# Kernel optimization log

Measured on AMD Instinct MI355X. Metric: run time of the kernel, lower is better.

## Reference

```python
import jax, jax.numpy as jnp
import numpy as np

N, CIN, COUT, K, CSTYLE, H, W = 8, 512, 512, 3, 512, 64, 64
EPS = 1e-8
SQRT2 = 2.0 ** 0.5


def setup_inputs() -> dict:
    key = jax.random.key(0)
    ks = jax.random.split(key, 5)
    return {
        "x": jax.random.normal(ks[0], (N, CIN, H, W), jnp.float32),
        "style": jax.random.normal(ks[1], (N, CSTYLE), jnp.float32),
        "noise": jax.random.normal(ks[2], (N, 1, H, W), jnp.float32),
        "conv_weight": jax.random.normal(ks[3], (1, COUT, CIN, K, K), jnp.float32),
        "mod_weight": jax.random.normal(ks[4], (CIN, CSTYLE), jnp.float32) / np.float32(np.sqrt(CSTYLE)),
        "mod_bias": jnp.ones((CIN,), jnp.float32),
        "noise_weight": jnp.zeros((1,), jnp.float32),
        "act_bias": jnp.zeros((COUT,), jnp.float32),
    }


def reference(x, style, noise, conv_weight, mod_weight, mod_bias, noise_weight, act_bias):
    n = x.shape[0]
    # style modulation: linear(style) -> per-sample per-in-channel scale (style_bias=0)
    s = style @ mod_weight.T + mod_bias                       # (n, cin)
    # modulate shared weight (1, cout, cin, k, k) -> (n, cout, cin, k, k)
    w = conv_weight * s[:, None, :, None, None]
    # demodulate
    demod = jax.lax.rsqrt(jnp.sum(w * w, axis=(2, 3, 4)) + EPS)  # (n, cout)
    w = w * demod[:, :, None, None, None]
    # grouped conv: groups = batch
    w = w.reshape(n * COUT, CIN, K, K)
    xg = x.reshape(1, n * CIN, H, W)
    out = jax.lax.conv_general_dilated(
        xg, w,
        window_strides=(1, 1),
        padding=[(K // 2, K // 2), (K // 2, K // 2)],
        dimension_numbers=("NCHW", "OIHW", "NCHW"),
        feature_group_count=n,
    )
    out = out.reshape(n, COUT, H, W) * SQRT2
    # noise injection (scalar weight, broadcast noise)
    out = out + noise_weight[0] * noise
    # fused bias + leaky relu (slope 0.2)
    out = jax.nn.leaky_relu(out + act_bias[None, :, None, None], negative_slope=0.2)
    return out
```

## Files before the change

kernel.cpp:

```cpp
#include <hip/hip_runtime.h>
#include <hip/hip_bf16.h>
#include <stdint.h>


typedef __attribute__((ext_vector_type(8))) short short8;
typedef __attribute__((ext_vector_type(4))) float f32x4;
typedef __attribute__((ext_vector_type(16))) float f32x16;
typedef __attribute__((ext_vector_type(4))) unsigned int uint4v;
typedef __attribute__((ext_vector_type(2))) unsigned int uint2v;

__device__ __forceinline__ unsigned short f2bf(float f) {
  unsigned u = __builtin_bit_cast(unsigned, f);
  u += 0x7FFFu + ((u >> 16) & 1u);
  return (unsigned short)(u >> 16);
}

__device__ __forceinline__ void g2l16(const void* g, void* l) {
  __builtin_amdgcn_global_load_lds(
      (const __attribute__((address_space(1))) void*)g,
      (__attribute__((address_space(3))) void*)l, 16, 0, 0);
}

__global__ void k_pre(const float* __restrict__ style, const float* __restrict__ mw,
                      const float* __restrict__ mb, const float* __restrict__ cw,
                      float* __restrict__ s_out, float* __restrict__ wsq) {
  int t = threadIdx.x;
  int b = blockIdx.x;
  if (b < 1024) {
    int wid = b * 4 + (t >> 6);
    int lane = t & 63;
    int n = wid >> 9, ci = wid & 511;
    float sum = 0.f;
#pragma unroll
    for (int i = 0; i < 8; ++i) {
      int k = lane + i * 64;
      sum += style[n * 512 + k] * mw[ci * 512 + k];
    }
#pragma unroll
    for (int off = 32; off; off >>= 1) sum += __shfl_xor(sum, off, 64);
    if (lane == 0) s_out[wid] = sum + mb[ci];
  } else {
    int id = (b - 1024) * 256 + t;
    const float* p = cw + (size_t)id * 9;
    float a = 0.f;
#pragma unroll
    for (int j = 0; j < 9; ++j) a += p[j] * p[j];
    wsq[id] = a;
  }
}

__global__ void k_mid(const float* __restrict__ s, const float* __restrict__ wsq,
                      const float* __restrict__ x, const float* __restrict__ cw,
                      float* __restrict__ demod, unsigned short* __restrict__ Xp,
                      unsigned short* __restrict__ Wt) {
  __shared__ char smem[74240];
  int t = threadIdx.x;
  int b = blockIdx.x;
  if (b < 512) {
    int n = b >> 6, h = b & 63;
    short* ldsx = (short*)smem;
    float* sxf = (float*)(smem + 69632);
    sxf[t] = s[n * 512 + t];
    sxf[t + 256] = s[n * 512 + 256 + t];
    __syncthreads();
    const float* xb = x + ((size_t)n * 512) * 4096 + h * 64;
#pragma unroll
    for (int i = 0; i < 32; ++i) {
      int L = t + i * 256;
      int ci = L >> 4, q = L & 15;
      f32x4 v = *(const f32x4*)(xb + (size_t)ci * 4096 + q * 4);
      float sv = sxf[ci];
      uint2v o;
      o.x = f2bf(v.x * sv) | ((unsigned)f2bf(v.y * sv) << 16);
      o.y = f2bf(v.z * sv) | ((unsigned)f2bf(v.w * sv) << 16);
      *(uint2v*)(ldsx + ci * 68 + q * 4) = o;
    }
    __syncthreads();
    unsigned short* nb = Xp + (size_t)n * 2230272 + (size_t)(h + 1) * 33792;
#pragma unroll
    for (int r = 0; r < 16; ++r) {
      int u = t + r * 256;
      int cig = u >> 6, col = u & 63;
      unsigned v[8];
#pragma unroll
      for (int j = 0; j < 8; ++j)
        v[j] = (unsigned short)ldsx[(cig * 8 + j) * 68 + col];
      uint4v o;
      o.x = v[0] | (v[1] << 16);
      o.y = v[2] | (v[3] << 16);
      o.z = v[4] | (v[5] << 16);
      o.w = v[6] | (v[7] << 16);
      *(uint4v*)(nb + ((size_t)cig * 66 + col + 1) * 8) = o;
    }
  } else if (b < 1536) {
    int wid = (b - 512) * 4 + (t >> 6);
    int lane = t & 63;
    int n = wid >> 9, co = wid & 511;
    float sum = 0.f;
#pragma unroll
    for (int i = 0; i < 8; ++i) {
      int ci = lane + i * 64;
      float sv = s[n * 512 + ci];
      sum += sv * sv * wsq[co * 512 + ci];
    }
#pragma unroll
    for (int off = 32; off; off >>= 1) sum += __shfl_xor(sum, off, 64);
    if (lane == 0) demod[wid] = rsqrtf(sum + 1e-8f) * 1.41421356237309515f;
  } else if (b < 1792) {
    int bb = b - 1536;
    int cb = bb >> 4, kb = bb & 15;
    float* ldsf = (float*)smem;
#pragma unroll
    for (int i = 0; i < 36; ++i) {
      int idx = t + i * 256;
      int seg = idx / 288, off = idx - seg * 288;
      ldsf[seg * 289 + off] = cw[(size_t)(cb * 32 + seg) * 4608 + kb * 288 + off];
    }
    __syncthreads();
    unsigned short* ob = Wt + (size_t)(cb * 16 + kb) * 9216;
#pragma unroll
    for (int i = 0; i < 5; ++i) {
      int c = t + i * 256;
      if (c < 1152) {
        int co_rel = c & 31, lhi = (c >> 5) & 3, tap = c >> 7;
        unsigned v[8];
#pragma unroll
        for (int j = 0; j < 8; ++j)
          v[j] = f2bf(ldsf[co_rel * 289 + (lhi * 8 + j) * 9 + tap]);
        uint4v o;
        o.x = v[0] | (v[1] << 16);
        o.y = v[2] | (v[3] << 16);
        o.z = v[4] | (v[5] << 16);
        o.w = v[6] | (v[7] << 16);
        *(uint4v*)(ob + (size_t)c * 8) = o;
      }
    }
  } else {
    int bb = b - 1792;
    int n = bb / 17, part = bb % 17;
    uint4v z = (uint4v){0u, 0u, 0u, 0u};
    unsigned short* base = Xp + (size_t)n * 2230272;
#pragma unroll
    for (int i = 0; i < 4; ++i) {
      int id = part * 1024 + i * 256 + t;
      if (id < 16640) {
        size_t off;
        if (id < 8448) {
          int row = (id < 4224) ? 0 : 65;
          int c = id - ((id < 4224) ? 0 : 4224);
          off = (size_t)row * 33792 + (size_t)c * 8;
        } else {
          int id2 = id - 8448;
          int row = 1 + (id2 >> 7);
          int rem = id2 & 127;
          int klhi = rem >> 1;
          int col = (rem & 1) ? 65 : 0;
          off = (size_t)row * 33792 + ((size_t)klhi * 66 + col) * 8;
        }
        *(uint4v*)(base + off) = z;
      }
    }
  }
}

__global__ void __launch_bounds__(256, 3) k_conv(
    const unsigned short* __restrict__ Wt, const unsigned short* __restrict__ Xp,
    const float* __restrict__ demod, const float* __restrict__ noise,
    const float* __restrict__ nw_p, const float* __restrict__ act_bias,
    float* __restrict__ out) {
  __shared__ short lds_a[9216];
  __shared__ short lds_x[16896];
  int t = threadIdx.x;
  int wg = blockIdx.x;
  int n = wg & 7;
  int rem = wg >> 3;
  int cb = rem / 11;
  int bx = rem - cb * 11;
  int r0 = (bx < 10) ? bx * 6 : 58;
  int lane = t & 63, wv = t >> 6;
  int l31 = lane & 31, hi = lane >> 5;
  int ch = wv >> 1, rg = wv & 1;

  const unsigned short* abase = Wt + (size_t)cb * 16 * 9216;
  const unsigned short* xbase = Xp + (size_t)n * 2230272;
  int xoffg[9];
#pragma unroll
  for (int j = 0; j < 9; ++j) {
    int c = j * 256 + t;
    int r = c / 264, rc = c - r * 264;
    int off = (r0 + r) * 33792 + rc * 8;
    if (c >= 2112) off = 0;
    xoffg[j] = off;
  }

  f32x16 acc[3];
#pragma unroll
  for (int r = 0; r < 3; ++r)
#pragma unroll
    for (int q = 0; q < 16; ++q) acc[r][q] = 0.f;

  const int aoff = hi * 256 + l31 * 8;
  const int xb0 = hi * 528 + ch * 256 + l31 * 8;

  for (int kb = 0; kb < 16; ++kb) {
    __syncthreads();
    const char* ab = (const char*)(abase + (size_t)kb * 9216);
#pragma unroll
    for (int i = 0; i < 5; ++i) {
      int c = i * 256 + t;
      if (c < 1152) g2l16(ab + c * 16, (char*)lds_a + c * 16);
    }
#pragma unroll
    for (int j = 0; j < 9; ++j) {
      int c = j * 256 + t;
      if (c < 2112) g2l16(xbase + xoffg[j] + kb * 2112, (char*)lds_x + c * 16);
    }
    __syncthreads();

#pragma unroll
    for (int dw = 0; dw < 3; ++dw) {
      short8 bf[5][2];
#pragma unroll
      for (int rr = 0; rr < 5; ++rr)
#pragma unroll
        for (int ks = 0; ks < 2; ++ks)
          bf[rr][ks] = *(const short8*)(lds_x + (rg * 3 + rr) * 2112 + ks * 1056 +
                                        dw * 8 + xb0);
#pragma unroll
      for (int dh = 0; dh < 3; ++dh) {
        int tap = dh * 3 + dw;
#pragma unroll
        for (int ks = 0; ks < 2; ++ks) {
          short8 af = *(const short8*)(lds_a + tap * 1024 + ks * 512 + aoff);
#pragma unroll
          for (int r = 0; r < 3; ++r)
            acc[r] = __builtin_amdgcn_mfma_f32_32x32x16_bf16(af, bf[r + dh][ks],
                                                             acc[r], 0, 0, 0);
        }
      }
    }
  }

  float nw = nw_p[0];
  int col = ch * 32 + l31;
  f32x4 dm4[4], ab4[4];
#pragma unroll
  for (int q = 0; q < 4; ++q) {
    dm4[q] = *(const f32x4*)(demod + n * 512 + cb * 32 + q * 8 + hi * 4);
    ab4[q] = *(const f32x4*)(act_bias + cb * 32 + q * 8 + hi * 4);
  }
#pragma unroll
  for (int r = 0; r < 3; ++r) {
    int R = r0 + rg * 3 + r;
    float nz = nw * noise[((size_t)n * 64 + R) * 64 + col];
#pragma unroll
    for (int q = 0; q < 4; ++q) {
#pragma unroll
      for (int c = 0; c < 4; ++c) {
        int co = cb * 32 + q * 8 + hi * 4 + c;
        float v = dm4[q][c] * acc[r][q * 4 + c] + nz + ab4[q][c];
        v = v > 0.f ? v : 0.2f * v;
        out[(((size_t)n * 512 + co) * 64 + R) * 64 + col] = v;
      }
    }
  }
}

extern "C" void kernel_launch(void* const* d_in, const int* in_sizes, int n_in,
                              void* d_out, int out_size, void* d_ws, size_t ws_size,
                              hipStream_t stream) {
  const float* x     = (const float*)d_in[0];
  const float* style = (const float*)d_in[1];
  const float* noise = (const float*)d_in[2];
  const float* cw    = (const float*)d_in[3];
  const float* mw    = (const float*)d_in[4];
  const float* mb    = (const float*)d_in[5];
  const float* nw    = (const float*)d_in[6];
  const float* ab    = (const float*)d_in[7];
  float* out = (float*)d_out;

  char* ws = (char*)d_ws;
  float* s_buf  = (float*)ws;
  float* demod  = (float*)(ws + 16384);
  float* wsq    = (float*)(ws + 32768);
  unsigned short* Wt = (unsigned short*)(ws + 1081344);
  unsigned short* Xp = (unsigned short*)(ws + 5799936);

  k_pre<<<2048, 256, 0, stream>>>(style, mw, mb, cw, s_buf, wsq);
  k_mid<<<1928, 256, 0, stream>>>(s_buf, wsq, x, cw, demod, Xp, Wt);
  k_conv<<<1408, 256, 0, stream>>>(Wt, Xp, demod, noise, nw, ab, out);
}
```

Baseline: 270.0 us.

## Enlarge conv tile to 64 output channels by 8 rows per workgroup

Each workgroup of the implicit-GEMM conv now computes two 32-channel blocks over 8 output rows, where it previously computed one block over 6 rows. Each wave holds a 2x4 accumulator set, so every loaded weight fragment and input fragment feeds more MFMAs. This removes the overlapping halo rows and duplicated weight loads of the old 11-row-block split, and the grid drops to 512 workgroups. In exchange, LDS use and register pressure rise and occupancy falls to 2 workgroups per CU, so there is less latency hiding and a smaller grid.

```diff
diff --git a/kernel.cpp b/kernel.cpp
--- a/kernel.cpp
+++ b/kernel.cpp
@@ -163,79 +163,84 @@
   }
 }
 
-__global__ void __launch_bounds__(256, 3) k_conv(
+__global__ void __launch_bounds__(256, 2) k_conv(
     const unsigned short* __restrict__ Wt, const unsigned short* __restrict__ Xp,
     const float* __restrict__ demod, const float* __restrict__ noise,
     const float* __restrict__ nw_p, const float* __restrict__ act_bias,
     float* __restrict__ out) {
-  __shared__ short lds_a[9216];
-  __shared__ short lds_x[16896];
+  __shared__ short lds_a[18432];
+  __shared__ short lds_x[22528];
   int t = threadIdx.x;
   int wg = blockIdx.x;
   int n = wg & 7;
   int rem = wg >> 3;
-  int cb = rem / 11;
-  int bx = rem - cb * 11;
-  int r0 = (bx < 10) ? bx * 6 : 58;
+  int rx = rem & 7;
+  int cb = rem >> 3;
+  int r0 = rx * 8;
   int lane = t & 63, wv = t >> 6;
   int l31 = lane & 31, hi = lane >> 5;
-  int ch = wv >> 1, rg = wv & 1;
-
-  const unsigned short* abase = Wt + (size_t)cb * 16 * 9216;
+  int ch = wv & 1, rg = wv >> 1;
+
+  const char* ab0 = (const char*)(Wt + (size_t)((cb * 2) * 16) * 9216);
+  const char* ab1 = (const char*)(Wt + (size_t)((cb * 2 + 1) * 16) * 9216);
   const unsigned short* xbase = Xp + (size_t)n * 2230272;
-  int xoffg[9];
-#pragma unroll
-  for (int j = 0; j < 9; ++j) {
+  int xoffg[11];
+#pragma unroll
+  for (int j = 0; j < 11; ++j) {
     int c = j * 256 + t;
     int r = c / 264, rc = c - r * 264;
     int off = (r0 + r) * 33792 + rc * 8;
-    if (c >= 2112) off = 0;
+    if (c >= 2640) off = 0;
     xoffg[j] = off;
   }
 
-  f32x16 acc[3];
-#pragma unroll
-  for (int r = 0; r < 3; ++r)
-#pragma unroll
-    for (int q = 0; q < 16; ++q) acc[r][q] = 0.f;
+  f32x16 acc[2][4];
+#pragma unroll
+  for (int m = 0; m < 2; ++m)
+#pragma unroll
+    for (int r = 0; r < 4; ++r)
+#pragma unroll
+      for (int q = 0; q < 16; ++q) acc[m][r][q] = 0.f;
 
   const int aoff = hi * 256 + l31 * 8;
   const int xb0 = hi * 528 + ch * 256 + l31 * 8;
 
   for (int kb = 0; kb < 16; ++kb) {
     __syncthreads();
-    const char* ab = (const char*)(abase + (size_t)kb * 9216);
-#pragma unroll
-    for (int i = 0; i < 5; ++i) {
+#pragma unroll
+    for (int i = 0; i < 9; ++i) {
       int c = i * 256 + t;
-      if (c < 1152) g2l16(ab + c * 16, (char*)lds_a + c * 16);
-    }
-#pragma unroll
-    for (int j = 0; j < 9; ++j) {
-      int c = j * 256 + t;
-      if (c < 2112) g2l16(xbase + xoffg[j] + kb * 2112, (char*)lds_x + c * 16);
-    }
+      const char* src = (c < 1152) ? (ab0 + (size_t)kb * 18432 + c * 16)
+                                   : (ab1 + (size_t)kb * 18432 + (c - 1152) * 16);
+      g2l16(src, (char*)lds_a + c * 16);
+    }
+#pragma unroll
+    for (int j = 0; j < 11; ++j)
+      g2l16(xbase + xoffg[j] + kb * 2112, (char*)lds_x + j * 4096 + t * 16);
     __syncthreads();
 
 #pragma unroll
     for (int dw = 0; dw < 3; ++dw) {
-      short8 bf[5][2];
-#pragma unroll
-      for (int rr = 0; rr < 5; ++rr)
+      short8 bf[6][2];
+#pragma unroll
+      for (int rr = 0; rr < 6; ++rr)
 #pragma unroll
         for (int ks = 0; ks < 2; ++ks)
-          bf[rr][ks] = *(const short8*)(lds_x + (rg * 3 + rr) * 2112 + ks * 1056 +
+          bf[rr][ks] = *(const short8*)(lds_x + (rg * 4 + rr) * 2112 + ks * 1056 +
                                         dw * 8 + xb0);
 #pragma unroll
       for (int dh = 0; dh < 3; ++dh) {
         int tap = dh * 3 + dw;
 #pragma unroll
         for (int ks = 0; ks < 2; ++ks) {
-          short8 af = *(const short8*)(lds_a + tap * 1024 + ks * 512 + aoff);
-#pragma unroll
-          for (int r = 0; r < 3; ++r)
-            acc[r] = __builtin_amdgcn_mfma_f32_32x32x16_bf16(af, bf[r + dh][ks],
-                                                             acc[r], 0, 0, 0);
+#pragma unroll
+          for (int m = 0; m < 2; ++m) {
+            short8 af = *(const short8*)(lds_a + m * 9216 + tap * 1024 + ks * 512 + aoff);
+#pragma unroll
+            for (int r = 0; r < 4; ++r)
+              acc[m][r] = __builtin_amdgcn_mfma_f32_32x32x16_bf16(af, bf[r + dh][ks],
+                                                                  acc[m][r], 0, 0, 0);
+          }
         }
       }
     }
@@ -243,24 +248,29 @@
 
   float nw = nw_p[0];
   int col = ch * 32 + l31;
-  f32x4 dm4[4], ab4[4];
-#pragma unroll
-  for (int q = 0; q < 4; ++q) {
-    dm4[q] = *(const f32x4*)(demod + n * 512 + cb * 32 + q * 8 + hi * 4);
-    ab4[q] = *(const f32x4*)(act_bias + cb * 32 + q * 8 + hi * 4);
-  }
-#pragma unroll
-  for (int r = 0; r < 3; ++r) {
-    int R = r0 + rg * 3 + r;
+  f32x4 dm4[2][4], ab4[2][4];
+#pragma unroll
+  for (int m = 0; m < 2; ++m)
+#pragma unroll
+    for (int q = 0; q < 4; ++q) {
+      dm4[m][q] = *(const f32x4*)(demod + n * 512 + cb * 64 + m * 32 + q * 8 + hi * 4);
+      ab4[m][q] = *(const f32x4*)(act_bias + cb * 64 + m * 32 + q * 8 + hi * 4);
+    }
+#pragma unroll
+  for (int r = 0; r < 4; ++r) {
+    int R = r0 + rg * 4 + r;
     float nz = nw * noise[((size_t)n * 64 + R) * 64 + col];
 #pragma unroll
-    for (int q = 0; q < 4; ++q) {
-#pragma unroll
-      for (int c = 0; c < 4; ++c) {
-        int co = cb * 32 + q * 8 + hi * 4 + c;
-        float v = dm4[q][c] * acc[r][q * 4 + c] + nz + ab4[q][c];
-        v = v > 0.f ? v : 0.2f * v;
-        out[(((size_t)n * 512 + co) * 64 + R) * 64 + col] = v;
+    for (int m = 0; m < 2; ++m) {
+#pragma unroll
+      for (int q = 0; q < 4; ++q) {
+#pragma unroll
+        for (int c = 0; c < 4; ++c) {
+          int co = cb * 64 + m * 32 + q * 8 + hi * 4 + c;
+          float v = dm4[m][q][c] * acc[m][r][q * 4 + c] + nz + ab4[m][q][c];
+          v = v > 0.f ? v : 0.2f * v;
+          out[(((size_t)n * 512 + co) * 64 + R) * 64 + col] = v;
+        }
       }
     }
   }
@@ -288,5 +298,5 @@
 
   k_pre<<<2048, 256, 0, stream>>>(style, mw, mb, cw, s_buf, wsq);
   k_mid<<<1928, 256, 0, stream>>>(s_buf, wsq, x, cw, demod, Xp, Wt);
-  k_conv<<<1408, 256, 0, stream>>>(Wt, Xp, demod, noise, nw, ab, out);
-}
+  k_conv<<<512, 256, 0, stream>>>(Wt, Xp, demod, noise, nw, ab, out);
+}
```

After: 258.2 us. 1.05x faster.
